# Performance work log

Hardware: AMD Instinct MI355X
Metric: run time of the kernel (lower is better)

## Reference

```python
import jax, jax.numpy as jnp
import numpy as np

B, C, H, W = 4, 256, 64, 64
G = 32          # GroupNorm groups
EPS = 1e-6


def setup_inputs() -> dict:
    key = jax.random.key(0)
    ks = jax.random.split(key, 6)
    inp = {
        "x": jax.random.normal(ks[0], (B, C, H, W), dtype=jnp.float32),
        "gamma": jnp.ones((C,), jnp.float32),
        "beta": jnp.zeros((C,), jnp.float32),
        "wq": jax.random.normal(ks[1], (C, C), jnp.float32) * 0.02,
        "bq": jnp.zeros((C,), jnp.float32),
        "wk": jax.random.normal(ks[2], (C, C), jnp.float32) * 0.02,
        "bk": jnp.zeros((C,), jnp.float32),
        "wv": jax.random.normal(ks[3], (C, C), jnp.float32) * 0.02,
        "bv": jnp.zeros((C,), jnp.float32),
        "wp": jax.random.normal(ks[4], (C, C), jnp.float32) * 0.02,
        "bp": jnp.zeros((C,), jnp.float32),
    }
    return inp


def _group_norm(x, gamma, beta):
    b, c, h, w = x.shape
    xs = x.reshape(b, G, c // G, h, w)
    mu = xs.mean(axis=(2, 3, 4), keepdims=True)
    var = xs.var(axis=(2, 3, 4), keepdims=True)  # biased, matches torch GroupNorm
    xn = ((xs - mu) * jax.lax.rsqrt(var + EPS)).reshape(b, c, h, w)
    return xn * gamma[None, :, None, None] + beta[None, :, None, None]


def _conv1x1(s, w, bias):
    # 1x1 conv == per-pixel channel matmul
    return jnp.einsum('oc,bchw->bohw', w, s) + bias[None, :, None, None]


def reference(x, gamma, beta, wq, bq, wk, bk, wv, bv, wp, bp):
    b, c, h, w = x.shape
    s = _group_norm(x, gamma, beta)
    q = _conv1x1(s, wq, bq).reshape(b, c, h * w)  # [B, C, N]
    k = _conv1x1(s, wk, bk).reshape(b, c, h * w)
    v = _conv1x1(s, wv, bv).reshape(b, c, h * w)
    # scores[b,i,j] = sum_c q[b,c,i] k[b,c,j], scaled by C^-1/2
    scores = jnp.einsum('bci,bcj->bij', q, k) * (c ** -0.5)
    attn = jax.nn.softmax(scores, axis=2)
    # h_[b,c,i] = sum_j v[b,c,j] attn[b,i,j]
    h_ = jnp.einsum('bij,bcj->bci', attn, v).reshape(b, c, h, w)
    h_ = _conv1x1(h_, wp, bp)
    return x + h_
```

## Files before the change

kernel.cpp:

```cpp
#include <hip/hip_runtime.h>

#define BB 4
#define CCH 256
#define NPIX 4096
#define EPS 1e-6f

typedef __attribute__((ext_vector_type(8))) short bf16x8;
typedef __attribute__((ext_vector_type(4))) float f32x4;

__device__ __forceinline__ unsigned short f2bf(float f) {
    return (unsigned short)((__float_as_uint(f) + 0x8000u) >> 16);
}
__device__ __forceinline__ float bf2f(unsigned short h) {
    return __uint_as_float((unsigned)h << 16);
}
__device__ __forceinline__ void gl2lds16(const void* g, void* l) {
    __builtin_amdgcn_global_load_lds(
        (const __attribute__((address_space(1))) unsigned int*)g,
        (__attribute__((address_space(3))) unsigned int*)l, 16, 0, 0);
}

__global__ __launch_bounds__(256) void gn_apply(const float* __restrict__ x,
                                                const float* __restrict__ gamma,
                                                const float* __restrict__ beta,
                                                unsigned short* __restrict__ sb) {
    int bg = blockIdx.x;
    int b = bg >> 5, g = bg & 31;
    const float4* x4 = (const float4*)(x + (size_t)(b * CCH + g * 8) * NPIX);
    float s = 0.f, ss = 0.f;
    for (int e = threadIdx.x; e < 8 * NPIX / 4; e += 256) {
        float4 v = x4[e];
        s += v.x + v.y + v.z + v.w;
        ss += v.x * v.x + v.y * v.y + v.z * v.z + v.w * v.w;
    }
    __shared__ float rs[256], rss[256];
    __shared__ float mean_s, rstd_s;
    rs[threadIdx.x] = s; rss[threadIdx.x] = ss;
    __syncthreads();
    for (int off = 128; off > 0; off >>= 1) {
        if (threadIdx.x < (unsigned)off) {
            rs[threadIdx.x] += rs[threadIdx.x + off];
            rss[threadIdx.x] += rss[threadIdx.x + off];
        }
        __syncthreads();
    }
    if (threadIdx.x == 0) {
        const float inv = 1.0f / (float)(8 * NPIX);
        float m = rs[0] * inv;
        float var = rss[0] * inv - m * m;
        mean_s = m;
        rstd_s = rsqrtf(var + EPS);
    }
    __syncthreads();
    float scale[8], shift[8];
#pragma unroll
    for (int ci = 0; ci < 8; ++ci) {
        float ga = gamma[g * 8 + ci], be = beta[g * 8 + ci];
        scale[ci] = rstd_s * ga;
        shift[ci] = be - mean_s * scale[ci];
    }
#pragma unroll 1
    for (int r = 0; r < 4; ++r) {
        int pq = r * 256 + threadIdx.x;
        __align__(16) unsigned short h[4][8];
#pragma unroll
        for (int ci = 0; ci < 8; ++ci) {
            float4 v = x4[ci * 1024 + pq];
            h[0][ci] = f2bf(v.x * scale[ci] + shift[ci]);
            h[1][ci] = f2bf(v.y * scale[ci] + shift[ci]);
            h[2][ci] = f2bf(v.z * scale[ci] + shift[ci]);
            h[3][ci] = f2bf(v.w * scale[ci] + shift[ci]);
        }
        size_t base = ((size_t)(b * NPIX + pq * 4) << 8) + g * 8;
#pragma unroll
        for (int p = 0; p < 4; ++p)
            *(uint4*)(sb + base + (size_t)p * 256) = *(const uint4*)h[p];
    }
}

__global__ __launch_bounds__(256) void wcvt(const float* __restrict__ wq,
                                            const float* __restrict__ wk,
                                            const float* __restrict__ wv,
                                            const float* __restrict__ wp,
                                            unsigned short* __restrict__ wb) {
    int e = blockIdx.x * 256 + threadIdx.x;
    const float* srcs[4] = {wp, wq, wk, wv};
#pragma unroll
    for (int m = 0; m < 4; ++m) {
        float4 v = ((const float4*)srcs[m])[e];
        ushort4 h;
        h.x = f2bf(v.x); h.y = f2bf(v.y); h.z = f2bf(v.z); h.w = f2bf(v.w);
        *(ushort4*)(wb + (size_t)m * 65536 + (size_t)e * 4) = h;
    }
}

__global__ __launch_bounds__(256) void qkv_mfma(
    const unsigned short* __restrict__ sb, const unsigned short* __restrict__ wb,
    const float* __restrict__ bq, const float* __restrict__ bk,
    const float* __restrict__ bv,
    unsigned short* __restrict__ qT, unsigned short* __restrict__ kT,
    unsigned short* __restrict__ vB) {
    __shared__ __align__(16) char lds[34816];
    const int tid = threadIdx.x, lane = tid & 63, w = tid >> 6;
    const int ln15 = lane & 15, q = lane >> 4;
    const int n0 = blockIdx.x * 128;
    const int co0 = blockIdx.y * 128;
    const int z = blockIdx.z;
    const unsigned short* wm = wb + (size_t)(z + 1) * 65536;
    const float* bias = (z == 0) ? bq : (z == 1) ? bk : bv;

    f32x4 acc[2][8];
#pragma unroll
    for (int i2 = 0; i2 < 2; ++i2)
#pragma unroll
        for (int nf = 0; nf < 8; ++nf) {
            acc[i2][nf][0] = 0.f; acc[i2][nf][1] = 0.f;
            acc[i2][nf][2] = 0.f; acc[i2][nf][3] = 0.f;
        }

#pragma unroll 1
    for (int kt = 0; kt < 4; ++kt) {
#pragma unroll
        for (int r = 0; r < 4; ++r) {
            int gch = r * 256 + tid;
            int row = gch >> 3, sidx = gch & 7;
            int cc = sidx ^ (row & 7);
            gl2lds16(sb + ((size_t)(n0 + row) << 8) + kt * 64 + cc * 8,
                     &lds[r * 4096 + w * 1024]);
            gl2lds16(wm + ((size_t)(co0 + row) << 8) + kt * 64 + cc * 8,
                     &lds[16384 + r * 4096 + w * 1024]);
        }
        __syncthreads();
#pragma unroll
        for (int kk = 0; kk < 2; ++kk) {
            int kc = kk * 4 + q;
            bf16x8 af[2], bf[8];
#pragma unroll
            for (int i2 = 0; i2 < 2; ++i2) {
                int row = w * 32 + i2 * 16 + ln15;
                af[i2] = *(const bf16x8*)&lds[row * 128 + ((kc ^ (row & 7)) << 4)];
            }
#pragma unroll
            for (int nf = 0; nf < 8; ++nf) {
                int row = nf * 16 + ln15;
                bf[nf] = *(const bf16x8*)&lds[16384 + row * 128 + ((kc ^ (row & 7)) << 4)];
            }
#pragma unroll
            for (int i2 = 0; i2 < 2; ++i2)
#pragma unroll
                for (int nf = 0; nf < 8; ++nf)
                    acc[i2][nf] = __builtin_amdgcn_mfma_f32_16x16x32_bf16(
                        af[i2], bf[nf], acc[i2][nf], 0, 0, 0);
        }
        __syncthreads();
    }

    float bias_l[8];
#pragma unroll
    for (int nf = 0; nf < 8; ++nf) bias_l[nf] = bias[co0 + nf * 16 + ln15];
    const float scl = (z == 0) ? 0.0625f : 1.0f;
    unsigned short* T = (unsigned short*)lds;
    if (z < 2) {
#pragma unroll
        for (int i2 = 0; i2 < 2; ++i2)
#pragma unroll
            for (int nf = 0; nf < 8; ++nf)
#pragma unroll
                for (int r = 0; r < 4; ++r) {
                    int n_l = w * 32 + i2 * 16 + q * 4 + r;
                    int co_l = nf * 16 + ln15;
                    T[n_l * 136 + co_l] = f2bf((acc[i2][nf][r] + bias_l[nf]) * scl);
                }
    } else {
#pragma unroll
        for (int i2 = 0; i2 < 2; ++i2)
#pragma unroll
            for (int nf = 0; nf < 8; ++nf)
#pragma unroll
                for (int r = 0; r < 4; ++r) {
                    int n_l = w * 32 + i2 * 16 + q * 4 + r;
                    int co_l = nf * 16 + ln15;
                    T[co_l * 136 + n_l] = f2bf(acc[i2][nf][r] + bias_l[nf]);
                }
    }
    __syncthreads();
    int row = tid >> 1, half = tid & 1;
    const uint4* src = (const uint4*)&T[row * 136 + half * 64];
    uint4* dst;
    if (z < 2) {
        unsigned short* qk = (z == 0) ? qT : kT;
        dst = (uint4*)(qk + ((size_t)(n0 + row) << 8) + co0 + half * 64);
    } else {
        int b2 = n0 >> 12, pix0 = n0 & 4095;
        dst = (uint4*)(vB + ((size_t)(b2 * CCH + co0 + row) << 12) + pix0 + half * 64);
    }
#pragma unroll
    for (int u = 0; u < 8; ++u) dst[u] = src[u];
}

__global__ __launch_bounds__(256, 2) void attn_mfma(
    const unsigned short* __restrict__ qT, const unsigned short* __restrict__ kT,
    const unsigned short* __restrict__ vB,
    unsigned short* __restrict__ pO, float* __restrict__ pml) {
    __shared__ __align__(16) char lds[73728];
    const int tid = threadIdx.x, lane = tid & 63, w = tid >> 6;
    const int ln15 = lane & 15, q = lane >> 4;
    const int bx = blockIdx.x;
    const int jh = bx & 1, b = (bx >> 1) & 3;
    const int itile = bx >> 3;
    const int i0 = itile * 64;
    const int jbase = jh * 2048;
    const size_t nb = (size_t)b * NPIX;
    const int wslot = 65536 + w * 2048;

#pragma unroll
    for (int t = 0; t < 8; ++t) {
        int gch = (w * 8 + t) * 64 + lane;
        int row = gch >> 5, sc = gch & 31;
        int cc = sc ^ (row & 7);
        gl2lds16(qT + ((nb + i0 + row) << 8) + cc * 8, &lds[(w * 8 + t) * 1024]);
    }
    __syncthreads();
    bf16x8 qf[8];
    {
        int row = w * 16 + ln15;
#pragma unroll
        for (int kb = 0; kb < 8; ++kb)
            qf[kb] = *(const bf16x8*)&lds[row * 512 + (((kb * 4 + q) ^ (row & 7)) << 4)];
    }
    __syncthreads();

    f32x4 O[16];
#pragma unroll
    for (int ns = 0; ns < 16; ++ns) {
        O[ns][0] = 0.f; O[ns][1] = 0.f; O[ns][2] = 0.f; O[ns][3] = 0.f;
    }
    float l_r[4];
#pragma unroll
    for (int r = 0; r < 4; ++r) l_r[r] = 0.f;

    {
        const int j0 = jbase;
#pragma unroll
        for (int t = 0; t < 8; ++t) {
            int gch = (w * 8 + t) * 64 + lane;
            int row = gch >> 5, sc = gch & 31;
            int cc = sc ^ (row & 7);
            gl2lds16(kT + ((nb + j0 + row) << 8) + cc * 8, &lds[(w * 8 + t) * 1024]);
        }
#pragma unroll
        for (int t = 0; t < 8; ++t) {
            int gch = (w * 8 + t) * 64 + lane;
            int c = gch >> 3, sv = gch & 7;
            int jc = sv ^ (c & 7);
            gl2lds16(vB + ((size_t)(b * CCH + c) << 12) + j0 + jc * 8,
                     &lds[32768 + (w * 8 + t) * 1024]);
        }
    }

#pragma unroll 1
    for (int jt = 0; jt < 32; ++jt) {
        asm volatile("s_waitcnt vmcnt(8)" ::: "memory");
        __builtin_amdgcn_s_barrier();

        f32x4 S[4];
#pragma unroll
        for (int js = 0; js < 4; ++js) {
            S[js][0] = 0.f; S[js][1] = 0.f; S[js][2] = 0.f; S[js][3] = 0.f;
        }
        __builtin_amdgcn_s_setprio(1);
#pragma unroll
        for (int kb = 0; kb < 8; ++kb)
#pragma unroll
            for (int js = 0; js < 4; ++js) {
                int jr = js * 16 + ln15;
                bf16x8 kf = *(const bf16x8*)&lds[jr * 512 + (((kb * 4 + q) ^ (jr & 7)) << 4)];
                S[js] = __builtin_amdgcn_mfma_f32_16x16x32_bf16(qf[kb], kf, S[js], 0, 0, 0);
            }
        __builtin_amdgcn_s_setprio(0);

        asm volatile("" ::: "memory");
        __builtin_amdgcn_s_barrier();
        if (jt < 31) {
            const int j0n = jbase + (jt + 1) * 64;
#pragma unroll
            for (int t = 0; t < 8; ++t) {
                int gch = (w * 8 + t) * 64 + lane;
                int row = gch >> 5, sc = gch & 31;
                int cc = sc ^ (row & 7);
                gl2lds16(kT + ((nb + j0n + row) << 8) + cc * 8,
                         &lds[(w * 8 + t) * 1024]);
            }
        }

#pragma unroll
        for (int r = 0; r < 4; ++r) {
            float p0 = __expf(S[0][r]), p1 = __expf(S[1][r]);
            float p2 = __expf(S[2][r]), p3 = __expf(S[3][r]);
            l_r[r] += (p0 + p1) + (p2 + p3);
            int il = q * 4 + r;
            float pv[4] = {p0, p1, p2, p3};
#pragma unroll
            for (int js = 0; js < 4; ++js) {
                int j = js * 16 + ln15;
                *(unsigned short*)&lds[wslot + il * 128 +
                    (((j >> 3) ^ (il & 7)) << 4) + ((j & 7) << 1)] = f2bf(pv[js]);
            }
        }
        asm volatile("s_waitcnt lgkmcnt(0)" ::: "memory");

        bf16x8 pf[2];
#pragma unroll
        for (int kf2 = 0; kf2 < 2; ++kf2)
            pf[kf2] = *(const bf16x8*)&lds[wslot + ln15 * 128 +
                                           (((kf2 * 4 + q) ^ (ln15 & 7)) << 4)];

        if (jt < 31) {
            asm volatile("s_waitcnt vmcnt(8)" ::: "memory");
        } else {
            asm volatile("s_waitcnt vmcnt(0)" ::: "memory");
        }
        __builtin_amdgcn_s_barrier();

        __builtin_amdgcn_s_setprio(1);
#pragma unroll
        for (int ns = 0; ns < 16; ++ns) {
            int c = ns * 16 + ln15;
            bf16x8 vf0 = *(const bf16x8*)&lds[32768 + c * 128 + ((q ^ (c & 7)) << 4)];
            bf16x8 vf1 = *(const bf16x8*)&lds[32768 + c * 128 + (((4 + q) ^ (c & 7)) << 4)];
            O[ns] = __builtin_amdgcn_mfma_f32_16x16x32_bf16(pf[0], vf0, O[ns], 0, 0, 0);
            O[ns] = __builtin_amdgcn_mfma_f32_16x16x32_bf16(pf[1], vf1, O[ns], 0, 0, 0);
        }
        __builtin_amdgcn_s_setprio(0);

        asm volatile("" ::: "memory");
        __builtin_amdgcn_s_barrier();
        if (jt < 31) {
            const int j0n = jbase + (jt + 1) * 64;
#pragma unroll
            for (int t = 0; t < 8; ++t) {
                int gch = (w * 8 + t) * 64 + lane;
                int c = gch >> 3, sv = gch & 7;
                int jc = sv ^ (c & 7);
                gl2lds16(vB + ((size_t)(b * CCH + c) << 12) + j0n + jc * 8,
                         &lds[32768 + (w * 8 + t) * 1024]);
            }
        }
    }

    size_t pbase = (size_t)bx * (64 * 256);
#pragma unroll
    for (int ns = 0; ns < 16; ++ns) {
        int c = ns * 16 + ln15;
#pragma unroll
        for (int r = 0; r < 4; ++r) {
            int i = w * 16 + q * 4 + r;
            pO[pbase + i * 256 + c] = f2bf(O[ns][r]);
        }
    }
#pragma unroll
    for (int r = 0; r < 4; ++r) {
        float l = l_r[r];
        l += __shfl_xor(l, 1);
        l += __shfl_xor(l, 2);
        l += __shfl_xor(l, 4);
        l += __shfl_xor(l, 8);
        l_r[r] = l;
    }
    if (ln15 == 0) {
#pragma unroll
        for (int r = 0; r < 4; ++r) {
            int i = w * 16 + q * 4 + r;
            pml[bx * 64 + i] = l_r[r];
        }
    }
}

__global__ __launch_bounds__(256) void attn_merge(
    const unsigned short* __restrict__ pO, const float* __restrict__ pml,
    unsigned short* __restrict__ hN) {
    int bid = blockIdx.x;
    int b = bid & 3, itile = bid >> 2;
    int bx0 = (itile << 3) | (b << 1), bx1 = bx0 | 1;
    __shared__ float fs[64];
    int t = threadIdx.x;
    if (t < 64) {
        float l0 = pml[bx0 * 64 + t], l1 = pml[bx1 * 64 + t];
        fs[t] = 1.0f / (l0 + l1);
    }
    __syncthreads();
    const unsigned short* p0 = pO + (size_t)bx0 * 16384;
    const unsigned short* p1 = pO + (size_t)bx1 * 16384;
    int i = t >> 2, cq = t & 3;
    float f = fs[i];
    size_t nrow = ((size_t)(b * NPIX + itile * 64 + i)) << 8;
#pragma unroll
    for (int p = 0; p < 16; ++p) {
        int c = p * 16 + cq * 4;
        ushort4 a = *(const ushort4*)&p0[i * 256 + c];
        ushort4 bb = *(const ushort4*)&p1[i * 256 + c];
        ushort4 h;
        h.x = f2bf((bf2f(a.x) + bf2f(bb.x)) * f);
        h.y = f2bf((bf2f(a.y) + bf2f(bb.y)) * f);
        h.z = f2bf((bf2f(a.z) + bf2f(bb.z)) * f);
        h.w = f2bf((bf2f(a.w) + bf2f(bb.w)) * f);
        *(ushort4*)&hN[nrow + c] = h;
    }
}

__global__ __launch_bounds__(256) void proj_mfma(
    const unsigned short* __restrict__ hN, const unsigned short* __restrict__ wb,
    const float* __restrict__ bp, const float* __restrict__ x,
    float* __restrict__ out) {
    __shared__ __align__(16) char lds[34816];
    const int tid = threadIdx.x, lane = tid & 63, w = tid >> 6;
    const int ln15 = lane & 15, q = lane >> 4;
    const int n0 = blockIdx.x * 128;
    const int co0 = blockIdx.y * 128;

    f32x4 acc[2][8];
#pragma unroll
    for (int i2 = 0; i2 < 2; ++i2)
#pragma unroll
        for (int nf = 0; nf < 8; ++nf) {
            acc[i2][nf][0] = 0.f; acc[i2][nf][1] = 0.f;
            acc[i2][nf][2] = 0.f; acc[i2][nf][3] = 0.f;
        }

#pragma unroll 1
    for (int kt = 0; kt < 4; ++kt) {
#pragma unroll
        for (int r = 0; r < 4; ++r) {
            int gch = r * 256 + tid;
            int row = gch >> 3, sidx = gch & 7;
            int cc = sidx ^ (row & 7);
            gl2lds16(hN + ((size_t)(n0 + row) << 8) + kt * 64 + cc * 8,
                     &lds[r * 4096 + w * 1024]);
            gl2lds16(wb + ((size_t)(co0 + row) << 8) + kt * 64 + cc * 8,
                     &lds[16384 + r * 4096 + w * 1024]);
        }
        __syncthreads();
#pragma unroll
        for (int kk = 0; kk < 2; ++kk) {
            int kc = kk * 4 + q;
            bf16x8 af[2], bf[8];
#pragma unroll
            for (int i2 = 0; i2 < 2; ++i2) {
                int row = w * 32 + i2 * 16 + ln15;
                af[i2] = *(const bf16x8*)&lds[row * 128 + ((kc ^ (row & 7)) << 4)];
            }
#pragma unroll
            for (int nf = 0; nf < 8; ++nf) {
                int row = nf * 16 + ln15;
                bf[nf] = *(const bf16x8*)&lds[16384 + row * 128 + ((kc ^ (row & 7)) << 4)];
            }
#pragma unroll
            for (int i2 = 0; i2 < 2; ++i2)
#pragma unroll
                for (int nf = 0; nf < 8; ++nf)
                    acc[i2][nf] = __builtin_amdgcn_mfma_f32_16x16x32_bf16(
                        af[i2], bf[nf], acc[i2][nf], 0, 0, 0);
        }
        __syncthreads();
    }

    unsigned short* T = (unsigned short*)lds;
#pragma unroll
    for (int i2 = 0; i2 < 2; ++i2)
#pragma unroll
        for (int nf = 0; nf < 8; ++nf)
#pragma unroll
            for (int r = 0; r < 4; ++r) {
                int n_l = w * 32 + i2 * 16 + q * 4 + r;
                int co_l = nf * 16 + ln15;
                T[co_l * 136 + n_l] = f2bf(acc[i2][nf][r]);
            }
    __syncthreads();
    int row = tid >> 1, half = tid & 1;
    int b2 = n0 >> 12, pix0 = n0 & 4095;
    float br = bp[co0 + row];
    size_t gidx = (((size_t)(b2 * CCH + co0 + row)) << 12) + pix0 + half * 64;
    const unsigned short* trow = &T[row * 136 + half * 64];
#pragma unroll
    for (int u = 0; u < 16; ++u) {
        float4 xv = *(const float4*)&x[gidx + u * 4];
        ushort4 tv = *(const ushort4*)&trow[u * 4];
        float4 o;
        o.x = xv.x + br + bf2f(tv.x);
        o.y = xv.y + br + bf2f(tv.y);
        o.z = xv.z + br + bf2f(tv.z);
        o.w = xv.w + br + bf2f(tv.w);
        *(float4*)&out[gidx + u * 4] = o;
    }
}

extern "C" void kernel_launch(void* const* d_in, const int* in_sizes, int n_in,
                              void* d_out, int out_size, void* d_ws, size_t ws_size,
                              hipStream_t stream) {
    const float* x     = (const float*)d_in[0];
    const float* gamma = (const float*)d_in[1];
    const float* beta  = (const float*)d_in[2];
    const float* wq    = (const float*)d_in[3];
    const float* bq    = (const float*)d_in[4];
    const float* wk    = (const float*)d_in[5];
    const float* bk    = (const float*)d_in[6];
    const float* wv    = (const float*)d_in[7];
    const float* bv    = (const float*)d_in[8];
    const float* wp    = (const float*)d_in[9];
    const float* bp    = (const float*)d_in[10];
    float* out = (float*)d_out;

    char* wsb = (char*)d_ws;
    unsigned short* sb  = (unsigned short*)wsb;
    unsigned short* hN  = sb;
    unsigned short* wb  = (unsigned short*)(wsb + 8388608);
    unsigned short* pO  = (unsigned short*)(wsb + 8912896);
    float*          pml = (float*)(wsb + 25690112);
    unsigned short* qT  = (unsigned short*)(wsb + 25952256);
    unsigned short* kT  = (unsigned short*)(wsb + 34340864);
    unsigned short* vB  = (unsigned short*)(wsb + 42729472);

    gn_apply<<<BB * 32, 256, 0, stream>>>(x, gamma, beta, sb);
    wcvt<<<64, 256, 0, stream>>>(wq, wk, wv, wp, wb);
    qkv_mfma<<<dim3(128, 2, 3), 256, 0, stream>>>(sb, wb, bq, bk, bv, qT, kT, vB);
    attn_mfma<<<512, 256, 0, stream>>>(qT, kT, vB, pO, pml);
    attn_merge<<<256, 256, 0, stream>>>(pO, pml, hN);
    proj_mfma<<<dim3(128, 2), 256, 0, stream>>>(hN, wb, bp, x, out);
}
```

Before: 232.9 us.

## Split attention key range four ways with smaller j-tiles for higher occupancy

The attention kernel is templated on the number of key-range splits (4 when the workspace is large enough, otherwise 2). The j-tile shrinks from 64 to 32, which halves LDS use and raises launch bounds to 4 blocks per CU. The merge kernel now sums NS partial outputs and normalisers. This adds parallelism and occupancy, at the cost of more partial-output traffic, more merge work, and more loop iterations and barriers per unit of work.

```diff
diff --git a/kernel.cpp b/kernel.cpp
--- a/kernel.cpp
+++ b/kernel.cpp
@@ -198,20 +198,24 @@
     for (int u = 0; u < 8; ++u) dst[u] = src[u];
 }
 
-__global__ __launch_bounds__(256, 2) void attn_mfma(
+template <int NS>
+__global__ __launch_bounds__(256, 4) void attn_mfma(
     const unsigned short* __restrict__ qT, const unsigned short* __restrict__ kT,
     const unsigned short* __restrict__ vB,
     unsigned short* __restrict__ pO, float* __restrict__ pml) {
-    __shared__ __align__(16) char lds[73728];
+    __shared__ __align__(16) char lds[36864];
     const int tid = threadIdx.x, lane = tid & 63, w = tid >> 6;
     const int ln15 = lane & 15, q = lane >> 4;
     const int bx = blockIdx.x;
-    const int jh = bx & 1, b = (bx >> 1) & 3;
-    const int itile = bx >> 3;
+    constexpr int LOGNS = (NS == 4) ? 2 : 1;
+    constexpr int NITER = 4096 / NS / 32;
+    const int jq = bx & (NS - 1);
+    const int b = (bx >> LOGNS) & 3;
+    const int itile = bx >> (LOGNS + 2);
     const int i0 = itile * 64;
-    const int jbase = jh * 2048;
+    const int jbase = jq * (4096 / NS);
     const size_t nb = (size_t)b * NPIX;
-    const int wslot = 65536 + w * 2048;
+    const int pslot = 32768 + w * 1024;
 
 #pragma unroll
     for (int t = 0; t < 8; ++t) {
@@ -242,37 +246,37 @@
     {
         const int j0 = jbase;
 #pragma unroll
-        for (int t = 0; t < 8; ++t) {
-            int gch = (w * 8 + t) * 64 + lane;
+        for (int t = 0; t < 4; ++t) {
+            int gch = (w * 4 + t) * 64 + lane;
             int row = gch >> 5, sc = gch & 31;
             int cc = sc ^ (row & 7);
-            gl2lds16(kT + ((nb + j0 + row) << 8) + cc * 8, &lds[(w * 8 + t) * 1024]);
-        }
-#pragma unroll
-        for (int t = 0; t < 8; ++t) {
-            int gch = (w * 8 + t) * 64 + lane;
-            int c = gch >> 3, sv = gch & 7;
-            int jc = sv ^ (c & 7);
+            gl2lds16(kT + ((nb + j0 + row) << 8) + cc * 8, &lds[(w * 4 + t) * 1024]);
+        }
+#pragma unroll
+        for (int t = 0; t < 4; ++t) {
+            int gch = (w * 4 + t) * 64 + lane;
+            int c = gch >> 2, sv = gch & 3;
+            int jc = sv ^ ((c >> 1) & 3);
             gl2lds16(vB + ((size_t)(b * CCH + c) << 12) + j0 + jc * 8,
-                     &lds[32768 + (w * 8 + t) * 1024]);
+                     &lds[16384 + (w * 4 + t) * 1024]);
         }
     }
 
 #pragma unroll 1
-    for (int jt = 0; jt < 32; ++jt) {
-        asm volatile("s_waitcnt vmcnt(8)" ::: "memory");
+    for (int jt = 0; jt < NITER; ++jt) {
+        asm volatile("s_waitcnt vmcnt(4)" ::: "memory");
         __builtin_amdgcn_s_barrier();
 
-        f32x4 S[4];
-#pragma unroll
-        for (int js = 0; js < 4; ++js) {
+        f32x4 S[2];
+#pragma unroll
+        for (int js = 0; js < 2; ++js) {
             S[js][0] = 0.f; S[js][1] = 0.f; S[js][2] = 0.f; S[js][3] = 0.f;
         }
         __builtin_amdgcn_s_setprio(1);
 #pragma unroll
         for (int kb = 0; kb < 8; ++kb)
 #pragma unroll
-            for (int js = 0; js < 4; ++js) {
+            for (int js = 0; js < 2; ++js) {
                 int jr = js * 16 + ln15;
                 bf16x8 kf = *(const bf16x8*)&lds[jr * 512 + (((kb * 4 + q) ^ (jr & 7)) << 4)];
                 S[js] = __builtin_amdgcn_mfma_f32_16x16x32_bf16(qf[kb], kf, S[js], 0, 0, 0);
@@ -281,42 +285,38 @@
 
         asm volatile("" ::: "memory");
         __builtin_amdgcn_s_barrier();
-        if (jt < 31) {
-            const int j0n = jbase + (jt + 1) * 64;
-#pragma unroll
-            for (int t = 0; t < 8; ++t) {
-                int gch = (w * 8 + t) * 64 + lane;
+        if (jt < NITER - 1) {
+            const int j0n = jbase + (jt + 1) * 32;
+#pragma unroll
+            for (int t = 0; t < 4; ++t) {
+                int gch = (w * 4 + t) * 64 + lane;
                 int row = gch >> 5, sc = gch & 31;
                 int cc = sc ^ (row & 7);
                 gl2lds16(kT + ((nb + j0n + row) << 8) + cc * 8,
-                         &lds[(w * 8 + t) * 1024]);
+                         &lds[(w * 4 + t) * 1024]);
             }
         }
 
 #pragma unroll
         for (int r = 0; r < 4; ++r) {
             float p0 = __expf(S[0][r]), p1 = __expf(S[1][r]);
-            float p2 = __expf(S[2][r]), p3 = __expf(S[3][r]);
-            l_r[r] += (p0 + p1) + (p2 + p3);
+            l_r[r] += p0 + p1;
             int il = q * 4 + r;
-            float pv[4] = {p0, p1, p2, p3};
-#pragma unroll
-            for (int js = 0; js < 4; ++js) {
+            float pv[2] = {p0, p1};
+#pragma unroll
+            for (int js = 0; js < 2; ++js) {
                 int j = js * 16 + ln15;
-                *(unsigned short*)&lds[wslot + il * 128 +
-                    (((j >> 3) ^ (il & 7)) << 4) + ((j & 7) << 1)] = f2bf(pv[js]);
+                *(unsigned short*)&lds[pslot + il * 64 +
+                    (((j >> 3) ^ ((il >> 1) & 3)) << 4) + ((j & 7) << 1)] = f2bf(pv[js]);
             }
         }
         asm volatile("s_waitcnt lgkmcnt(0)" ::: "memory");
 
-        bf16x8 pf[2];
-#pragma unroll
-        for (int kf2 = 0; kf2 < 2; ++kf2)
-            pf[kf2] = *(const bf16x8*)&lds[wslot + ln15 * 128 +
-                                           (((kf2 * 4 + q) ^ (ln15 & 7)) << 4)];
-
-        if (jt < 31) {
-            asm volatile("s_waitcnt vmcnt(8)" ::: "memory");
+        bf16x8 pf = *(const bf16x8*)&lds[pslot + ln15 * 64 +
+                                         ((q ^ ((ln15 >> 1) & 3)) << 4)];
+
+        if (jt < NITER - 1) {
+            asm volatile("s_waitcnt vmcnt(4)" ::: "memory");
         } else {
             asm volatile("s_waitcnt vmcnt(0)" ::: "memory");
         }
@@ -326,24 +326,22 @@
 #pragma unroll
         for (int ns = 0; ns < 16; ++ns) {
             int c = ns * 16 + ln15;
-            bf16x8 vf0 = *(const bf16x8*)&lds[32768 + c * 128 + ((q ^ (c & 7)) << 4)];
-            bf16x8 vf1 = *(const bf16x8*)&lds[32768 + c * 128 + (((4 + q) ^ (c & 7)) << 4)];
-            O[ns] = __builtin_amdgcn_mfma_f32_16x16x32_bf16(pf[0], vf0, O[ns], 0, 0, 0);
-            O[ns] = __builtin_amdgcn_mfma_f32_16x16x32_bf16(pf[1], vf1, O[ns], 0, 0, 0);
+            bf16x8 vf = *(const bf16x8*)&lds[16384 + c * 64 + ((q ^ ((c >> 1) & 3)) << 4)];
+            O[ns] = __builtin_amdgcn_mfma_f32_16x16x32_bf16(pf, vf, O[ns], 0, 0, 0);
         }
         __builtin_amdgcn_s_setprio(0);
 
         asm volatile("" ::: "memory");
         __builtin_amdgcn_s_barrier();
-        if (jt < 31) {
-            const int j0n = jbase + (jt + 1) * 64;
-#pragma unroll
-            for (int t = 0; t < 8; ++t) {
-                int gch = (w * 8 + t) * 64 + lane;
-                int c = gch >> 3, sv = gch & 7;
-                int jc = sv ^ (c & 7);
+        if (jt < NITER - 1) {
+            const int j0n = jbase + (jt + 1) * 32;
+#pragma unroll
+            for (int t = 0; t < 4; ++t) {
+                int gch = (w * 4 + t) * 64 + lane;
+                int c = gch >> 2, sv = gch & 3;
+                int jc = sv ^ ((c >> 1) & 3);
                 gl2lds16(vB + ((size_t)(b * CCH + c) << 12) + j0n + jc * 8,
-                         &lds[32768 + (w * 8 + t) * 1024]);
+                         &lds[16384 + (w * 4 + t) * 1024]);
             }
         }
     }
@@ -376,34 +374,37 @@
     }
 }
 
+template <int NS>
 __global__ __launch_bounds__(256) void attn_merge(
     const unsigned short* __restrict__ pO, const float* __restrict__ pml,
     unsigned short* __restrict__ hN) {
     int bid = blockIdx.x;
     int b = bid & 3, itile = bid >> 2;
-    int bx0 = (itile << 3) | (b << 1), bx1 = bx0 | 1;
+    int bx0 = (itile * 4 + b) * NS;
     __shared__ float fs[64];
     int t = threadIdx.x;
     if (t < 64) {
-        float l0 = pml[bx0 * 64 + t], l1 = pml[bx1 * 64 + t];
-        fs[t] = 1.0f / (l0 + l1);
-    }
-    __syncthreads();
-    const unsigned short* p0 = pO + (size_t)bx0 * 16384;
-    const unsigned short* p1 = pO + (size_t)bx1 * 16384;
+        float l = 0.f;
+#pragma unroll
+        for (int s = 0; s < NS; ++s) l += pml[(bx0 + s) * 64 + t];
+        fs[t] = 1.0f / l;
+    }
+    __syncthreads();
     int i = t >> 2, cq = t & 3;
     float f = fs[i];
     size_t nrow = ((size_t)(b * NPIX + itile * 64 + i)) << 8;
 #pragma unroll
     for (int p = 0; p < 16; ++p) {
         int c = p * 16 + cq * 4;
-        ushort4 a = *(const ushort4*)&p0[i * 256 + c];
-        ushort4 bb = *(const ushort4*)&p1[i * 256 + c];
+        float o0 = 0.f, o1 = 0.f, o2 = 0.f, o3 = 0.f;
+#pragma unroll
+        for (int s = 0; s < NS; ++s) {
+            ushort4 a = *(const ushort4*)&pO[(size_t)(bx0 + s) * 16384 + i * 256 + c];
+            o0 += bf2f(a.x); o1 += bf2f(a.y); o2 += bf2f(a.z); o3 += bf2f(a.w);
+        }
         ushort4 h;
-        h.x = f2bf((bf2f(a.x) + bf2f(bb.x)) * f);
-        h.y = f2bf((bf2f(a.y) + bf2f(bb.y)) * f);
-        h.z = f2bf((bf2f(a.z) + bf2f(bb.z)) * f);
-        h.w = f2bf((bf2f(a.w) + bf2f(bb.w)) * f);
+        h.x = f2bf(o0 * f); h.y = f2bf(o1 * f);
+        h.z = f2bf(o2 * f); h.w = f2bf(o3 * f);
         *(ushort4*)&hN[nrow + c] = h;
     }
 }
@@ -510,20 +511,27 @@
     const float* bp    = (const float*)d_in[10];
     float* out = (float*)d_out;
 
-    char* wsb = (char*)d_ws;
-    unsigned short* sb  = (unsigned short*)wsb;
+    const int NS = (ws_size >= 67895296u) ? 4 : 2;
+
+    char* p = (char*)d_ws;
+    unsigned short* sb  = (unsigned short*)p; p += 8388608;
     unsigned short* hN  = sb;
-    unsigned short* wb  = (unsigned short*)(wsb + 8388608);
-    unsigned short* pO  = (unsigned short*)(wsb + 8912896);
-    float*          pml = (float*)(wsb + 25690112);
-    unsigned short* qT  = (unsigned short*)(wsb + 25952256);
-    unsigned short* kT  = (unsigned short*)(wsb + 34340864);
-    unsigned short* vB  = (unsigned short*)(wsb + 42729472);
+    unsigned short* wb  = (unsigned short*)p; p += 524288;
+    unsigned short* pO  = (unsigned short*)p; p += (size_t)NS * 8388608;
+    float*          pml = (float*)p;          p += (size_t)NS * 65536;
+    unsigned short* qT  = (unsigned short*)p; p += 8388608;
+    unsigned short* kT  = (unsigned short*)p; p += 8388608;
+    unsigned short* vB  = (unsigned short*)p;
 
     gn_apply<<<BB * 32, 256, 0, stream>>>(x, gamma, beta, sb);
     wcvt<<<64, 256, 0, stream>>>(wq, wk, wv, wp, wb);
     qkv_mfma<<<dim3(128, 2, 3), 256, 0, stream>>>(sb, wb, bq, bk, bv, qT, kT, vB);
-    attn_mfma<<<512, 256, 0, stream>>>(qT, kT, vB, pO, pml);
-    attn_merge<<<256, 256, 0, stream>>>(pO, pml, hN);
+    if (NS == 4) {
+        attn_mfma<4><<<1024, 256, 0, stream>>>(qT, kT, vB, pO, pml);
+        attn_merge<4><<<256, 256, 0, stream>>>(pO, pml, hN);
+    } else {
+        attn_mfma<2><<<512, 256, 0, stream>>>(qT, kT, vB, pO, pml);
+        attn_merge<2><<<256, 256, 0, stream>>>(pO, pml, hN);
+    }
     proj_mfma<<<dim3(128, 2), 256, 0, stream>>>(hN, wb, bp, x, out);
 }
```

After: 416.8 us. 1.79x slower.

## Double query rows per attention block and split keys four ways

Applied to the files above, without the earlier changes.

Each attention workgroup now handles 128 query rows, two 16-row groups per wave, instead of 64. The key dimension is split into four chunks of 1024 rather than two halves, which keeps the grid at 512 blocks. Each K/V tile loaded into LDS now feeds twice as many MFMAs, cutting global load traffic and barrier overhead per unit of work. The costs are more accumulator registers (occupancy may drop under launch_bounds 2), a larger LDS allocation, and a merge kernel that reads four partial results per row instead of two, doubling the partial-output buffer.

```diff
diff --git a/kernel.cpp b/kernel.cpp
--- a/kernel.cpp
+++ b/kernel.cpp
@@ -202,42 +202,50 @@
     const unsigned short* __restrict__ qT, const unsigned short* __restrict__ kT,
     const unsigned short* __restrict__ vB,
     unsigned short* __restrict__ pO, float* __restrict__ pml) {
-    __shared__ __align__(16) char lds[73728];
+    __shared__ __align__(16) char lds[81920];
     const int tid = threadIdx.x, lane = tid & 63, w = tid >> 6;
     const int ln15 = lane & 15, q = lane >> 4;
     const int bx = blockIdx.x;
-    const int jh = bx & 1, b = (bx >> 1) & 3;
-    const int itile = bx >> 3;
-    const int i0 = itile * 64;
-    const int jbase = jh * 2048;
+    const int xk = bx & 7;
+    const int b = xk >> 1, jqhi = xk & 1;
+    const int outer = bx >> 3;
+    const int jqlo = outer & 1, itile = outer >> 1;
+    const int i0 = itile * 128;
+    const int jbase = (jqhi * 2 + jqlo) * 1024;
     const size_t nb = (size_t)b * NPIX;
-    const int wslot = 65536 + w * 2048;
-
-#pragma unroll
-    for (int t = 0; t < 8; ++t) {
-        int gch = (w * 8 + t) * 64 + lane;
+    const int pslot = 65536 + w * 4096;
+
+#pragma unroll
+    for (int t = 0; t < 16; ++t) {
+        int gch = (w * 16 + t) * 64 + lane;
         int row = gch >> 5, sc = gch & 31;
         int cc = sc ^ (row & 7);
-        gl2lds16(qT + ((nb + i0 + row) << 8) + cc * 8, &lds[(w * 8 + t) * 1024]);
-    }
-    __syncthreads();
-    bf16x8 qf[8];
-    {
-        int row = w * 16 + ln15;
+        gl2lds16(qT + ((nb + i0 + row) << 8) + cc * 8, &lds[(w * 16 + t) * 1024]);
+    }
+    __syncthreads();
+    bf16x8 qf[2][8];
+#pragma unroll
+    for (int ig = 0; ig < 2; ++ig) {
+        int row = w * 32 + ig * 16 + ln15;
 #pragma unroll
         for (int kb = 0; kb < 8; ++kb)
-            qf[kb] = *(const bf16x8*)&lds[row * 512 + (((kb * 4 + q) ^ (row & 7)) << 4)];
-    }
-    __syncthreads();
-
-    f32x4 O[16];
-#pragma unroll
-    for (int ns = 0; ns < 16; ++ns) {
-        O[ns][0] = 0.f; O[ns][1] = 0.f; O[ns][2] = 0.f; O[ns][3] = 0.f;
-    }
-    float l_r[4];
-#pragma unroll
-    for (int r = 0; r < 4; ++r) l_r[r] = 0.f;
+            qf[ig][kb] = *(const bf16x8*)&lds[row * 512 + (((kb * 4 + q) ^ (row & 7)) << 4)];
+    }
+    __syncthreads();
+
+    f32x4 O[2][16];
+#pragma unroll
+    for (int ig = 0; ig < 2; ++ig)
+#pragma unroll
+        for (int ns = 0; ns < 16; ++ns) {
+            O[ig][ns][0] = 0.f; O[ig][ns][1] = 0.f;
+            O[ig][ns][2] = 0.f; O[ig][ns][3] = 0.f;
+        }
+    float l_r[2][4];
+#pragma unroll
+    for (int ig = 0; ig < 2; ++ig)
+#pragma unroll
+        for (int r = 0; r < 4; ++r) l_r[ig][r] = 0.f;
 
     {
         const int j0 = jbase;
@@ -259,15 +267,18 @@
     }
 
 #pragma unroll 1
-    for (int jt = 0; jt < 32; ++jt) {
+    for (int jt = 0; jt < 16; ++jt) {
         asm volatile("s_waitcnt vmcnt(8)" ::: "memory");
         __builtin_amdgcn_s_barrier();
 
-        f32x4 S[4];
-#pragma unroll
-        for (int js = 0; js < 4; ++js) {
-            S[js][0] = 0.f; S[js][1] = 0.f; S[js][2] = 0.f; S[js][3] = 0.f;
-        }
+        f32x4 S[2][4];
+#pragma unroll
+        for (int ig = 0; ig < 2; ++ig)
+#pragma unroll
+            for (int js = 0; js < 4; ++js) {
+                S[ig][js][0] = 0.f; S[ig][js][1] = 0.f;
+                S[ig][js][2] = 0.f; S[ig][js][3] = 0.f;
+            }
         __builtin_amdgcn_s_setprio(1);
 #pragma unroll
         for (int kb = 0; kb < 8; ++kb)
@@ -275,13 +286,14 @@
             for (int js = 0; js < 4; ++js) {
                 int jr = js * 16 + ln15;
                 bf16x8 kf = *(const bf16x8*)&lds[jr * 512 + (((kb * 4 + q) ^ (jr & 7)) << 4)];
-                S[js] = __builtin_amdgcn_mfma_f32_16x16x32_bf16(qf[kb], kf, S[js], 0, 0, 0);
+                S[0][js] = __builtin_amdgcn_mfma_f32_16x16x32_bf16(qf[0][kb], kf, S[0][js], 0, 0, 0);
+                S[1][js] = __builtin_amdgcn_mfma_f32_16x16x32_bf16(qf[1][kb], kf, S[1][js], 0, 0, 0);
             }
         __builtin_amdgcn_s_setprio(0);
 
         asm volatile("" ::: "memory");
         __builtin_amdgcn_s_barrier();
-        if (jt < 31) {
+        if (jt < 15) {
             const int j0n = jbase + (jt + 1) * 64;
 #pragma unroll
             for (int t = 0; t < 8; ++t) {
@@ -294,28 +306,32 @@
         }
 
 #pragma unroll
-        for (int r = 0; r < 4; ++r) {
-            float p0 = __expf(S[0][r]), p1 = __expf(S[1][r]);
-            float p2 = __expf(S[2][r]), p3 = __expf(S[3][r]);
-            l_r[r] += (p0 + p1) + (p2 + p3);
-            int il = q * 4 + r;
-            float pv[4] = {p0, p1, p2, p3};
-#pragma unroll
-            for (int js = 0; js < 4; ++js) {
-                int j = js * 16 + ln15;
-                *(unsigned short*)&lds[wslot + il * 128 +
-                    (((j >> 3) ^ (il & 7)) << 4) + ((j & 7) << 1)] = f2bf(pv[js]);
-            }
-        }
+        for (int ig = 0; ig < 2; ++ig)
+#pragma unroll
+            for (int r = 0; r < 4; ++r) {
+                float p0 = __expf(S[ig][0][r]), p1 = __expf(S[ig][1][r]);
+                float p2 = __expf(S[ig][2][r]), p3 = __expf(S[ig][3][r]);
+                l_r[ig][r] += (p0 + p1) + (p2 + p3);
+                int il = ig * 16 + q * 4 + r;
+                float pv[4] = {p0, p1, p2, p3};
+#pragma unroll
+                for (int js = 0; js < 4; ++js) {
+                    int j = js * 16 + ln15;
+                    *(unsigned short*)&lds[pslot + il * 128 +
+                        (((j >> 3) ^ (il & 7)) << 4) + ((j & 7) << 1)] = f2bf(pv[js]);
+                }
+            }
         asm volatile("s_waitcnt lgkmcnt(0)" ::: "memory");
 
-        bf16x8 pf[2];
-#pragma unroll
-        for (int kf2 = 0; kf2 < 2; ++kf2)
-            pf[kf2] = *(const bf16x8*)&lds[wslot + ln15 * 128 +
-                                           (((kf2 * 4 + q) ^ (ln15 & 7)) << 4)];
-
-        if (jt < 31) {
+        bf16x8 pf[2][2];
+#pragma unroll
+        for (int ig = 0; ig < 2; ++ig)
+#pragma unroll
+            for (int kf2 = 0; kf2 < 2; ++kf2)
+                pf[ig][kf2] = *(const bf16x8*)&lds[pslot + (ig * 16 + ln15) * 128 +
+                                                  (((kf2 * 4 + q) ^ (ln15 & 7)) << 4)];
+
+        if (jt < 15) {
             asm volatile("s_waitcnt vmcnt(8)" ::: "memory");
         } else {
             asm volatile("s_waitcnt vmcnt(0)" ::: "memory");
@@ -328,14 +344,16 @@
             int c = ns * 16 + ln15;
             bf16x8 vf0 = *(const bf16x8*)&lds[32768 + c * 128 + ((q ^ (c & 7)) << 4)];
             bf16x8 vf1 = *(const bf16x8*)&lds[32768 + c * 128 + (((4 + q) ^ (c & 7)) << 4)];
-            O[ns] = __builtin_amdgcn_mfma_f32_16x16x32_bf16(pf[0], vf0, O[ns], 0, 0, 0);
-            O[ns] = __builtin_amdgcn_mfma_f32_16x16x32_bf16(pf[1], vf1, O[ns], 0, 0, 0);
+            O[0][ns] = __builtin_amdgcn_mfma_f32_16x16x32_bf16(pf[0][0], vf0, O[0][ns], 0, 0, 0);
+            O[0][ns] = __builtin_amdgcn_mfma_f32_16x16x32_bf16(pf[0][1], vf1, O[0][ns], 0, 0, 0);
+            O[1][ns] = __builtin_amdgcn_mfma_f32_16x16x32_bf16(pf[1][0], vf0, O[1][ns], 0, 0, 0);
+            O[1][ns] = __builtin_amdgcn_mfma_f32_16x16x32_bf16(pf[1][1], vf1, O[1][ns], 0, 0, 0);
         }
         __builtin_amdgcn_s_setprio(0);
 
         asm volatile("" ::: "memory");
         __builtin_amdgcn_s_barrier();
-        if (jt < 31) {
+        if (jt < 15) {
             const int j0n = jbase + (jt + 1) * 64;
 #pragma unroll
             for (int t = 0; t < 8; ++t) {
@@ -348,62 +366,67 @@
         }
     }
 
-    size_t pbase = (size_t)bx * (64 * 256);
-#pragma unroll
-    for (int ns = 0; ns < 16; ++ns) {
-        int c = ns * 16 + ln15;
+    size_t pbase = (size_t)bx * (128 * 256);
+#pragma unroll
+    for (int ig = 0; ig < 2; ++ig)
+#pragma unroll
+        for (int ns = 0; ns < 16; ++ns) {
+            int c = ns * 16 + ln15;
+#pragma unroll
+            for (int r = 0; r < 4; ++r) {
+                int i = w * 32 + ig * 16 + q * 4 + r;
+                pO[pbase + i * 256 + c] = f2bf(O[ig][ns][r]);
+            }
+        }
+#pragma unroll
+    for (int ig = 0; ig < 2; ++ig)
 #pragma unroll
         for (int r = 0; r < 4; ++r) {
-            int i = w * 16 + q * 4 + r;
-            pO[pbase + i * 256 + c] = f2bf(O[ns][r]);
-        }
-    }
-#pragma unroll
-    for (int r = 0; r < 4; ++r) {
-        float l = l_r[r];
-        l += __shfl_xor(l, 1);
-        l += __shfl_xor(l, 2);
-        l += __shfl_xor(l, 4);
-        l += __shfl_xor(l, 8);
-        l_r[r] = l;
-    }
-    if (ln15 == 0) {
-#pragma unroll
-        for (int r = 0; r < 4; ++r) {
-            int i = w * 16 + q * 4 + r;
-            pml[bx * 64 + i] = l_r[r];
-        }
-    }
+            float l = l_r[ig][r];
+            l += __shfl_xor(l, 1);
+            l += __shfl_xor(l, 2);
+            l += __shfl_xor(l, 4);
+            l += __shfl_xor(l, 8);
+            if (ln15 == 0) {
+                int i = w * 32 + ig * 16 + q * 4 + r;
+                pml[bx * 128 + i] = l;
+            }
+        }
 }
 
 __global__ __launch_bounds__(256) void attn_merge(
     const unsigned short* __restrict__ pO, const float* __restrict__ pml,
     unsigned short* __restrict__ hN) {
     int bid = blockIdx.x;
-    int b = bid & 3, itile = bid >> 2;
-    int bx0 = (itile << 3) | (b << 1), bx1 = bx0 | 1;
+    int b = bid & 3, itile = (bid >> 2) & 31, ih = (bid >> 7) & 1;
+    int base = itile * 16 + b * 2;
+    const int offs[4] = {0, 1, 8, 9};
     __shared__ float fs[64];
     int t = threadIdx.x;
     if (t < 64) {
-        float l0 = pml[bx0 * 64 + t], l1 = pml[bx1 * 64 + t];
-        fs[t] = 1.0f / (l0 + l1);
-    }
-    __syncthreads();
-    const unsigned short* p0 = pO + (size_t)bx0 * 16384;
-    const unsigned short* p1 = pO + (size_t)bx1 * 16384;
+        float l = 0.f;
+#pragma unroll
+        for (int s = 0; s < 4; ++s)
+            l += pml[(base + offs[s]) * 128 + ih * 64 + t];
+        fs[t] = 1.0f / l;
+    }
+    __syncthreads();
     int i = t >> 2, cq = t & 3;
     float f = fs[i];
-    size_t nrow = ((size_t)(b * NPIX + itile * 64 + i)) << 8;
+    int row = ih * 64 + i;
+    size_t nrow = ((size_t)(b * NPIX + itile * 128 + row)) << 8;
 #pragma unroll
     for (int p = 0; p < 16; ++p) {
         int c = p * 16 + cq * 4;
-        ushort4 a = *(const ushort4*)&p0[i * 256 + c];
-        ushort4 bb = *(const ushort4*)&p1[i * 256 + c];
+        float o0 = 0.f, o1 = 0.f, o2 = 0.f, o3 = 0.f;
+#pragma unroll
+        for (int s = 0; s < 4; ++s) {
+            ushort4 a = *(const ushort4*)&pO[(size_t)(base + offs[s]) * 32768 + row * 256 + c];
+            o0 += bf2f(a.x); o1 += bf2f(a.y); o2 += bf2f(a.z); o3 += bf2f(a.w);
+        }
         ushort4 h;
-        h.x = f2bf((bf2f(a.x) + bf2f(bb.x)) * f);
-        h.y = f2bf((bf2f(a.y) + bf2f(bb.y)) * f);
-        h.z = f2bf((bf2f(a.z) + bf2f(bb.z)) * f);
-        h.w = f2bf((bf2f(a.w) + bf2f(bb.w)) * f);
+        h.x = f2bf(o0 * f); h.y = f2bf(o1 * f);
+        h.z = f2bf(o2 * f); h.w = f2bf(o3 * f);
         *(ushort4*)&hN[nrow + c] = h;
     }
 }
@@ -510,15 +533,15 @@
     const float* bp    = (const float*)d_in[10];
     float* out = (float*)d_out;
 
-    char* wsb = (char*)d_ws;
-    unsigned short* sb  = (unsigned short*)wsb;
+    char* p = (char*)d_ws;
+    unsigned short* sb  = (unsigned short*)p; p += 8388608;
     unsigned short* hN  = sb;
-    unsigned short* wb  = (unsigned short*)(wsb + 8388608);
-    unsigned short* pO  = (unsigned short*)(wsb + 8912896);
-    float*          pml = (float*)(wsb + 25690112);
-    unsigned short* qT  = (unsigned short*)(wsb + 25952256);
-    unsigned short* kT  = (unsigned short*)(wsb + 34340864);
-    unsigned short* vB  = (unsigned short*)(wsb + 42729472);
+    unsigned short* wb  = (unsigned short*)p; p += 524288;
+    unsigned short* pO  = (unsigned short*)p; p += 33554432;
+    float*          pml = (float*)p;          p += 262144;
+    unsigned short* qT  = (unsigned short*)p; p += 8388608;
+    unsigned short* kT  = (unsigned short*)p; p += 8388608;
+    unsigned short* vB  = (unsigned short*)p;
 
     gn_apply<<<BB * 32, 256, 0, stream>>>(x, gamma, beta, sb);
     wcvt<<<64, 256, 0, stream>>>(wq, wk, wv, wp, wb);
```

After: 503.9 us. +116.3%, slower.
